# Performance work log

Measured on AMD Instinct MI355X. Metric: run time of the kernel, lower is better.

The kernel has to match this reference:

```python
import jax, jax.numpy as jnp
import numpy as np

T, Z, Y, X = 16, 16, 16, 16
NS, NC = 4, 3
D = NS * NC  # 12 internal (spin*color) components
DIAG = 4.5   # 4 + mass
OUT_PARITY = 0


def _r_masks():
    t = jnp.arange(T).reshape(T, 1, 1, 1, 1)
    z = jnp.arange(Z).reshape(1, Z, 1, 1, 1)
    y = jnp.arange(Y).reshape(1, 1, Y, 1, 1)
    r = (t + z + y + OUT_PARITY) % 2
    r = jnp.broadcast_to(r, (T, Z, Y, X // 2, D))
    return r == 1, r == 0  # fwd mask, bwd mask


def _cmatvec(Kr, Ki, vr, vi):
    # complex (K) @ (v) per site; K: [T,Z,Y,X/2,D,D], v: [T,Z,Y,X/2,D]
    ar = jnp.einsum('tzyxij,tzyxj->tzyxi', Kr, vr) - jnp.einsum('tzyxij,tzyxj->tzyxi', Ki, vi)
    ai = jnp.einsum('tzyxij,tzyxj->tzyxi', Kr, vi) + jnp.einsum('tzyxij,tzyxj->tzyxi', Ki, vr)
    return ar, ai


def setup_inputs() -> dict:
    key = jax.random.key(0)
    ks = jax.random.split(key, 6)
    shp_psi = (T, Z, Y, X // 2, NS, NC)
    shp_K = (4, T, Z, Y, X // 2, D, D)
    return {
        'psi_re': jax.random.normal(ks[0], shp_psi, dtype=jnp.float32),
        'psi_im': jax.random.normal(ks[1], shp_psi, dtype=jnp.float32),
        'K_fwd_re': jax.random.normal(ks[2], shp_K, dtype=jnp.float32),
        'K_fwd_im': jax.random.normal(ks[3], shp_K, dtype=jnp.float32),
        'K_bwd_re': jax.random.normal(ks[4], shp_K, dtype=jnp.float32),
        'K_bwd_im': jax.random.normal(ks[5], shp_K, dtype=jnp.float32),
    }


def reference(psi_re, psi_im, K_fwd_re, K_fwd_im, K_bwd_re, K_bwd_im):
    pr = psi_re.reshape(T, Z, Y, X // 2, D)
    pi = psi_im.reshape(T, Z, Y, X // 2, D)
    mask_f, mask_b = _r_masks()
    out_re = DIAG * pr
    out_im = DIAG * pi
    for mu in range(4):
        ax = mu  # ldim = mu - 5 on a rank-5 tensor == axis mu
        if mu < 3:
            pf_re = jnp.roll(pr, -1, axis=ax); pf_im = jnp.roll(pi, -1, axis=ax)
            pb_re = jnp.roll(pr, 1, axis=ax); pb_im = jnp.roll(pi, 1, axis=ax)
        else:
            # staggered X hop on the half-lattice, selected by parity masks
            pf_re = jnp.where(mask_f, jnp.roll(pr, -1, axis=ax), pr)
            pf_im = jnp.where(mask_f, jnp.roll(pi, -1, axis=ax), pi)
            pb_re = jnp.where(mask_b, jnp.roll(pr, 1, axis=ax), pr)
            pb_im = jnp.where(mask_b, jnp.roll(pi, 1, axis=ax), pi)
        cf_re, cf_im = _cmatvec(K_fwd_re[mu], K_fwd_im[mu], pf_re, pf_im)
        cb_re, cb_im = _cmatvec(K_bwd_re[mu], K_bwd_im[mu], pb_re, pb_im)
        out_re = out_re - 0.5 * (cf_re + cb_re)
        out_im = out_im - 0.5 * (cf_im + cb_im)
    return (out_re.reshape(T, Z, Y, X // 2, NS, NC),
            out_im.reshape(T, Z, Y, X // 2, NS, NC))
```

## Files before the change

kernel.cpp:

```cpp
#include <hip/hip_runtime.h>

#define TD 16
#define ZD 16
#define YD 16
#define XH 8
#define DD 12
#define NSITES (TD*ZD*YD*XH)
#define SPB 16
#define THREADS (SPB*DD)
#define DIAG 4.5f
#define VSTRIDE 100
#define MU_STRIDE (NSITES*144)

__device__ __forceinline__ void cdot4(const float4 kr, const float4 ki,
                                      const float4 vr, const float4 vi,
                                      float& sr, float& si) {
    sr = fmaf(kr.x, vr.x, sr); sr = fmaf(-ki.x, vi.x, sr);
    si = fmaf(kr.x, vi.x, si); si = fmaf(ki.x, vr.x, si);
    sr = fmaf(kr.y, vr.y, sr); sr = fmaf(-ki.y, vi.y, sr);
    si = fmaf(kr.y, vi.y, si); si = fmaf(ki.y, vr.y, si);
    sr = fmaf(kr.z, vr.z, sr); sr = fmaf(-ki.z, vi.z, sr);
    si = fmaf(kr.z, vi.z, si); si = fmaf(ki.z, vr.z, si);
    sr = fmaf(kr.w, vr.w, sr); sr = fmaf(-ki.w, vi.w, sr);
    si = fmaf(kr.w, vi.w, si); si = fmaf(ki.w, vr.w, si);
}

__global__ __launch_bounds__(THREADS, 4) void hop_kernel(
    const float* __restrict__ psi_re, const float* __restrict__ psi_im,
    const float* __restrict__ K_fwd_re, const float* __restrict__ K_fwd_im,
    const float* __restrict__ K_bwd_re, const float* __restrict__ K_bwd_im,
    float* __restrict__ out_re, float* __restrict__ out_im)
{
    __shared__ float vre[SPB][VSTRIDE];
    __shared__ float vim[SPB][VSTRIDE];

    const int tid   = threadIdx.x;
    const int site0 = blockIdx.x * SPB;

    const int jj  = tid % 12;
    const int scb = tid / 12;
    const int cc  = scb & 7;
    const int sb  = scb >> 3;

    const int dt = (cc == 0) - (cc == 1);
    const int dz = (cc == 2) - (cc == 3);
    const int dy = (cc == 4) - (cc == 5);

    float tr[8], ti[8];
    int   dst[8];
    #pragma unroll
    for (int k = 0; k < 8; ++k) {
        const int s  = sb + 2 * k;
        const int sg = site0 + s;
        const int x = sg & 7, y = (sg >> 3) & 15, z = (sg >> 7) & 15, t = (sg >> 11) & 15;
        const int r = (t + z + y) & 1;
        int dx = 0;
        if (cc == 6) dx =  (r == 1);
        if (cc == 7) dx = -(r == 0);
        const int nt = (t + dt) & 15, nz = (z + dz) & 15,
                  ny = (y + dy) & 15, nx = (x + dx) & 7;
        const int n = ((nt * 16 + nz) * 16 + ny) * 8 + nx;
        const int a = n * 12 + jj;
        tr[k]  = psi_re[a];
        ti[k]  = psi_im[a];
        dst[k] = s * VSTRIDE + cc * 12 + jj;
    }
    #pragma unroll
    for (int k = 0; k < 8; ++k) {
        ((float*)vre)[dst[k]] = tr[k];
        ((float*)vim)[dst[k]] = ti[k];
    }
    __syncthreads();

    const int s      = scb;
    const int i      = jj;
    const int site   = site0 + s;
    const int rowoff = site * 144 + i * 12;

    const float pr_c = psi_re[site * 12 + i];
    const float pi_c = psi_im[site * 12 + i];
    float o_re = DIAG * pr_c;
    float o_im = DIAG * pi_c;

    #define KR(c) ((const float4*)((((c) & 1) ? K_bwd_re : K_fwd_re) + ((c) >> 1) * MU_STRIDE + rowoff))
    #define KI(c) ((const float4*)((((c) & 1) ? K_bwd_im : K_fwd_im) + ((c) >> 1) * MU_STRIDE + rowoff))

    float4 cr0 = KR(0)[0], cr1 = KR(0)[1], cr2 = KR(0)[2];
    float4 ci0 = KI(0)[0], ci1 = KI(0)[1], ci2 = KI(0)[2];

    #pragma unroll
    for (int c = 0; c < 8; ++c) {
        float4 nr0, nr1, nr2, ni0, ni1, ni2;
        if (c < 7) {
            nr0 = KR(c + 1)[0]; nr1 = KR(c + 1)[1]; nr2 = KR(c + 1)[2];
            ni0 = KI(c + 1)[0]; ni1 = KI(c + 1)[1]; ni2 = KI(c + 1)[2];
        }
        const float4* v4r = (const float4*)&vre[s][c * 12];
        const float4* v4i = (const float4*)&vim[s][c * 12];
        const float4 vr0 = v4r[0], vr1 = v4r[1], vr2 = v4r[2];
        const float4 vi0 = v4i[0], vi1 = v4i[1], vi2 = v4i[2];
        float sr = 0.f, si = 0.f;
        cdot4(cr0, ci0, vr0, vi0, sr, si);
        cdot4(cr1, ci1, vr1, vi1, sr, si);
        cdot4(cr2, ci2, vr2, vi2, sr, si);
        o_re -= 0.5f * sr;
        o_im -= 0.5f * si;
        if (c < 7) { cr0 = nr0; cr1 = nr1; cr2 = nr2; ci0 = ni0; ci1 = ni1; ci2 = ni2; }
    }

    out_re[site * 12 + i] = o_re;
    out_im[site * 12 + i] = o_im;
}

extern "C" void kernel_launch(void* const* d_in, const int* in_sizes, int n_in,
                              void* d_out, int out_size, void* d_ws, size_t ws_size,
                              hipStream_t stream) {
    const float* psi_re   = (const float*)d_in[0];
    const float* psi_im   = (const float*)d_in[1];
    const float* K_fwd_re = (const float*)d_in[2];
    const float* K_fwd_im = (const float*)d_in[3];
    const float* K_bwd_re = (const float*)d_in[4];
    const float* K_bwd_im = (const float*)d_in[5];
    float* out_re = (float*)d_out;
    float* out_im = out_re + (out_size / 2);

    hop_kernel<<<NSITES / SPB, THREADS, 0, stream>>>(
        psi_re, psi_im, K_fwd_re, K_fwd_im, K_bwd_re, K_bwd_im, out_re, out_im);
}
```

Measured before the change: 283.2 us.

## Stream K matrices into per-wave double-buffered LDS ring via global_load_lds

Hop-matrix loads no longer go through per-thread float4 register prefetches. Each wave now issues coalesced 16-byte direct global-to-LDS DMA loads into its own double-buffered ring slot, syncs with explicit vmcnt waits, and reads its rows back from LDS for the complex dot products. The center psi loads are also hoisted ahead of the neighbor LDS stores. The aim is better coalescing and more bytes in flight on a latency-bound stream. In exchange, LDS per block grows to roughly 49 KB, which can cap blocks per CU, and the launch-bounds occupancy hint drops from 4 to 2.

```diff
diff --git a/kernel.cpp b/kernel.cpp
--- a/kernel.cpp
+++ b/kernel.cpp
@@ -1,16 +1,21 @@
 #include <hip/hip_runtime.h>
 
-#define TD 16
-#define ZD 16
-#define YD 16
-#define XH 8
 #define DD 12
-#define NSITES (TD*ZD*YD*XH)
+#define NSITES 32768
 #define SPB 16
-#define THREADS (SPB*DD)
+#define THREADS 192
 #define DIAG 4.5f
 #define VSTRIDE 100
 #define MU_STRIDE (NSITES*144)
+#define SLOT_BYTES 6144
+#define WAVE_RING  (2*SLOT_BYTES)
+
+typedef __attribute__((address_space(3))) unsigned int       lds_u32_t;
+typedef __attribute__((address_space(1))) const unsigned int gbl_u32_t;
+
+__device__ __forceinline__ void dma16(const float* gp, unsigned char* lp) {
+    __builtin_amdgcn_global_load_lds((gbl_u32_t*)gp, (lds_u32_t*)lp, 16, 0, 0);
+}
 
 __device__ __forceinline__ void cdot4(const float4 kr, const float4 ki,
                                       const float4 vr, const float4 vi,
@@ -25,23 +30,25 @@
     si = fmaf(kr.w, vi.w, si); si = fmaf(ki.w, vr.w, si);
 }
 
-__global__ __launch_bounds__(THREADS, 4) void hop_kernel(
+__global__ __launch_bounds__(THREADS, 2) void hop_kernel(
     const float* __restrict__ psi_re, const float* __restrict__ psi_im,
     const float* __restrict__ K_fwd_re, const float* __restrict__ K_fwd_im,
     const float* __restrict__ K_bwd_re, const float* __restrict__ K_bwd_im,
     float* __restrict__ out_re, float* __restrict__ out_im)
 {
-    __shared__ float vre[SPB][VSTRIDE];
-    __shared__ float vim[SPB][VSTRIDE];
+    __shared__ alignas(16) unsigned char kring[3 * WAVE_RING];
+    __shared__ alignas(16) float vre[SPB][VSTRIDE];
+    __shared__ alignas(16) float vim[SPB][VSTRIDE];
 
     const int tid   = threadIdx.x;
     const int site0 = blockIdx.x * SPB;
+    const int wave  = tid >> 6;
+    const int lane  = tid & 63;
 
     const int jj  = tid % 12;
     const int scb = tid / 12;
     const int cc  = scb & 7;
     const int sb  = scb >> 3;
-
     const int dt = (cc == 0) - (cc == 1);
     const int dz = (cc == 2) - (cc == 3);
     const int dy = (cc == 4) - (cc == 5);
@@ -60,11 +67,17 @@
         const int nt = (t + dt) & 15, nz = (z + dz) & 15,
                   ny = (y + dy) & 15, nx = (x + dx) & 7;
         const int n = ((nt * 16 + nz) * 16 + ny) * 8 + nx;
-        const int a = n * 12 + jj;
-        tr[k]  = psi_re[a];
-        ti[k]  = psi_im[a];
+        tr[k]  = psi_re[n * 12 + jj];
+        ti[k]  = psi_im[n * 12 + jj];
         dst[k] = s * VSTRIDE + cc * 12 + jj;
     }
+
+    const int s    = scb;
+    const int i    = jj;
+    const int site = site0 + s;
+    const float pr_c = psi_re[site * 12 + i];
+    const float pi_c = psi_im[site * 12 + i];
+
     #pragma unroll
     for (int k = 0; k < 8; ++k) {
         ((float*)vre)[dst[k]] = tr[k];
@@ -72,41 +85,42 @@
     }
     __syncthreads();
 
-    const int s      = scb;
-    const int i      = jj;
-    const int site   = site0 + s;
-    const int rowoff = site * 144 + i * 12;
-
-    const float pr_c = psi_re[site * 12 + i];
-    const float pi_c = psi_im[site * 12 + i];
     float o_re = DIAG * pr_c;
     float o_im = DIAG * pi_c;
 
-    #define KR(c) ((const float4*)((((c) & 1) ? K_bwd_re : K_fwd_re) + ((c) >> 1) * MU_STRIDE + rowoff))
-    #define KI(c) ((const float4*)((((c) & 1) ? K_bwd_im : K_fwd_im) + ((c) >> 1) * MU_STRIDE + rowoff))
+    unsigned char* wring = kring + wave * WAVE_RING;
+    const int gw = site0 * 144 + wave * 768 + lane * 4;
 
-    float4 cr0 = KR(0)[0], cr1 = KR(0)[1], cr2 = KR(0)[2];
-    float4 ci0 = KI(0)[0], ci1 = KI(0)[1], ci2 = KI(0)[2];
+    #define ISSUE(c) do { \
+        const float* _kr = (((c) & 1) ? K_bwd_re : K_fwd_re) + ((c) >> 1) * MU_STRIDE + gw; \
+        const float* _ki = (((c) & 1) ? K_bwd_im : K_fwd_im) + ((c) >> 1) * MU_STRIDE + gw; \
+        unsigned char* _sp = wring + ((c) & 1) * SLOT_BYTES; \
+        dma16(_kr,       _sp);                dma16(_ki,       _sp + 3072); \
+        dma16(_kr + 256, _sp + 1024);         dma16(_ki + 256, _sp + 3072 + 1024); \
+        dma16(_kr + 512, _sp + 2048);         dma16(_ki + 512, _sp + 3072 + 2048); \
+    } while (0)
+
+    ISSUE(0);
 
     #pragma unroll
     for (int c = 0; c < 8; ++c) {
-        float4 nr0, nr1, nr2, ni0, ni1, ni2;
-        if (c < 7) {
-            nr0 = KR(c + 1)[0]; nr1 = KR(c + 1)[1]; nr2 = KR(c + 1)[2];
-            ni0 = KI(c + 1)[0]; ni1 = KI(c + 1)[1]; ni2 = KI(c + 1)[2];
-        }
+        __builtin_amdgcn_sched_barrier(0);
+        if (c < 7) ISSUE(c + 1);
+        if (c < 7) asm volatile("s_waitcnt vmcnt(6)" ::: "memory");
+        else       asm volatile("s_waitcnt vmcnt(0)" ::: "memory");
+        const unsigned char* sp = wring + (c & 1) * SLOT_BYTES;
+        const float4* kr4 = (const float4*)(sp + lane * 48);
+        const float4* ki4 = (const float4*)(sp + 3072 + lane * 48);
         const float4* v4r = (const float4*)&vre[s][c * 12];
         const float4* v4i = (const float4*)&vim[s][c * 12];
-        const float4 vr0 = v4r[0], vr1 = v4r[1], vr2 = v4r[2];
-        const float4 vi0 = v4i[0], vi1 = v4i[1], vi2 = v4i[2];
         float sr = 0.f, si = 0.f;
-        cdot4(cr0, ci0, vr0, vi0, sr, si);
-        cdot4(cr1, ci1, vr1, vi1, sr, si);
-        cdot4(cr2, ci2, vr2, vi2, sr, si);
+        cdot4(kr4[0], ki4[0], v4r[0], v4i[0], sr, si);
+        cdot4(kr4[1], ki4[1], v4r[1], v4i[1], sr, si);
+        cdot4(kr4[2], ki4[2], v4r[2], v4i[2], sr, si);
         o_re -= 0.5f * sr;
         o_im -= 0.5f * si;
-        if (c < 7) { cr0 = nr0; cr1 = nr1; cr2 = nr2; ci0 = ni0; ci1 = ni1; ci2 = ni2; }
     }
+    #undef ISSUE
 
     out_re[site * 12 + i] = o_re;
     out_im[site * 12 + i] = o_im;
```

New measurement: 272.2 us. -3.9%, faster.
